# Performance work log

Hardware: AMD Instinct MI355X
Metric: run time of the kernel (lower is better)

Reference implementation:

```python
import jax, jax.numpy as jnp
import numpy as np

TEMPERATURE = 0.07
SIM_THRESHOLD = 0.5


def setup_inputs() -> dict:
    key = jax.random.key(0)
    k1, k2 = jax.random.split(key)
    features = jax.random.normal(k1, (4096, 2, 128), dtype=jnp.float32)
    labels = jax.random.randint(k2, (4096, 100), 0, 2).astype(jnp.float32)
    return {"features": features, "labels": labels}


def reference(features, labels):
    B, V, D = features.shape

    # label Jaccard similarity -> positive/negative masks [B, B]
    intersection = labels @ labels.T
    row_sum = jnp.sum(labels, axis=1, keepdims=True)
    union = row_sum + row_sum.T - intersection
    similarity = intersection / (union + 1e-6)
    positive_mask = (similarity >= SIM_THRESHOLD).astype(jnp.float32)
    negative_mask = 1.0 - positive_mask

    # torch.cat(torch.unbind(features, dim=1), dim=0) -> [V*B, D] (view-major)
    contrast_feature = jnp.transpose(features, (1, 0, 2)).reshape(V * B, D)
    dot_similarities = (contrast_feature @ contrast_feature.T) / TEMPERATURE  # [VB, VB]

    # numerical stability: subtract detached row max over the FULL row
    logits_max = jax.lax.stop_gradient(jnp.max(dot_similarities, axis=1, keepdims=True))
    logits = dot_similarities - logits_max

    # only the top-left [B, B] block is ever indexed by the original loop
    e = jnp.exp(logits[:B, :B])
    pos_sum = jnp.sum(e * positive_mask, axis=1)  # [B]
    neg_sum = jnp.sum(e * negative_mask, axis=1)  # [B]

    has_pos = jnp.sum(positive_mask, axis=1) > 0  # rows with >=1 positive
    pos_safe = jnp.where(has_pos, pos_sum, 1.0)
    den_safe = jnp.where(has_pos, pos_sum + neg_sum, 1.0)
    per_row = -jnp.log(pos_safe / den_safe)

    count = jnp.sum(has_pos.astype(jnp.float32))
    loss = jnp.sum(jnp.where(has_pos, per_row, 0.0)) / jnp.maximum(count, 1.0)
    return loss
```

## Files before the change

kernel.cpp:

```cpp
#include <hip/hip_runtime.h>
#include <math.h>

#define B_ROWS 4096
#define DIM 128
#define LBL 100
#define NCT 32

typedef __attribute__((ext_vector_type(8))) short bf16x8;
typedef __attribute__((ext_vector_type(4))) float f32x4;

__device__ __forceinline__ unsigned f2bf(float x) {
  union { float f; unsigned u; } a; a.f = x;
  unsigned r = a.u + 0x7fffu + ((a.u >> 16) & 1u);
  return r >> 16;
}

__device__ __forceinline__ void lds_dma16(void* l, const void* g) {
  __builtin_amdgcn_global_load_lds(
      (const __attribute__((address_space(1))) void*)g,
      (__attribute__((address_space(3))) void*)l, 16, 0, 0);
}

__global__ void pack_kernel(const float* __restrict__ feat,
                            uint4* __restrict__ cf,
                            float* __restrict__ accum) {
  if (blockIdx.x == 0 && threadIdx.x < 2) accum[threadIdx.x] = 0.0f;
  int g = blockIdx.x * 256 + threadIdx.x;
  int tile = g >> 11, rem = g & 2047;
  int r = rem >> 4, kc = rem & 15;
  const float* src = feat + ((size_t)(tile * 128 + r)) * 256 + kc * 8;
  float4 a = *(const float4*)src;
  float4 b = *(const float4*)(src + 4);
  uint4 ov;
  ov.x = f2bf(a.x) | (f2bf(a.y) << 16);
  ov.y = f2bf(a.z) | (f2bf(a.w) << 16);
  ov.z = f2bf(b.x) | (f2bf(b.y) << 16);
  ov.w = f2bf(b.z) | (f2bf(b.w) << 16);
  cf[(size_t)tile * 2048 + kc * 128 + (r ^ kc)] = ov;
}

__global__ void seedlabel_kernel(const float* __restrict__ feat,
                                 const float* __restrict__ labels,
                                 uint4* __restrict__ Lb,
                                 int* __restrict__ rsv,
                                 float* __restrict__ seedRaw) {
  int w = (int)((blockIdx.x * blockDim.x + threadIdx.x) >> 6);
  int lane = threadIdx.x & 63;
  const float2* src = (const float2*)(feat + (size_t)w * 256);
  float2 f = src[lane];
  float b0 = __uint_as_float(f2bf(f.x) << 16);
  float b1 = __uint_as_float(f2bf(f.y) << 16);
  float s = b0 * b0 + b1 * b1;
  #pragma unroll
  for (int off = 32; off >= 1; off >>= 1) s += __shfl_xor(s, off);
  float x0 = labels[(size_t)w * LBL + lane];
  float x1 = (lane < LBL - 64) ? labels[(size_t)w * LBL + 64 + lane] : 0.0f;
  unsigned long long m0 = __ballot(x0 != 0.0f);
  unsigned long long m1 = __ballot(x1 != 0.0f);
  if (lane == 0) {
    Lb[w] = make_uint4((unsigned)m0, (unsigned)(m0 >> 32),
                       (unsigned)m1, (unsigned)(m1 >> 32));
    rsv[w] = __popcll(m0) + __popcll(m1);
    seedRaw[w] = s - 0.15f;
  }
}

__launch_bounds__(256, 2)
__global__ void main_kernel(const uint4* __restrict__ cf,
                            const uint4* __restrict__ Lb,
                            const int* __restrict__ rsv,
                            const float* __restrict__ seedRaw,
                            float2* __restrict__ part) {
  __shared__ uint4 As[2048];
  __shared__ uint4 Bs[2048];
  __shared__ uint4 cLb[128];
  __shared__ uint4 rLb[128];
  __shared__ int   cRs[128];
  __shared__ int   rRs[128];
  __shared__ float sS[128];
  const int tid = threadIdx.x;
  const int lane = tid & 63;
  const int l15 = lane & 15;
  const int quad = lane >> 4;
  const int wave = tid >> 6;
  const int wi = (wave & 1) * 64;
  const int wj = (wave >> 1) * 64;
  const int rowBase = blockIdx.x * 128;
  const int colBase = blockIdx.y * 128;
  const float invT = 1.0f / 0.07f;

  #pragma unroll
  for (int it = 0; it < 8; ++it) {
    int flat = it * 256 + tid;
    lds_dma16(&As[flat], &cf[(size_t)blockIdx.x * 2048 + flat]);
    lds_dma16(&Bs[flat], &cf[(size_t)blockIdx.y * 2048 + flat]);
  }
  if (tid < 128) {
    cLb[tid] = Lb[colBase + tid];
    cRs[tid] = rsv[colBase + tid];
    sS[tid] = seedRaw[rowBase + tid];
  } else {
    int t = tid - 128;
    rLb[t] = Lb[rowBase + t];
    rRs[t] = rsv[rowBase + t];
  }
  __syncthreads();

  float srow[16];
  #pragma unroll
  for (int ti = 0; ti < 4; ++ti)
    #pragma unroll
    for (int r = 0; r < 4; ++r)
      srow[ti * 4 + r] = sS[wi + ti * 16 + quad * 4 + r];

  const bf16x8* Asv = (const bf16x8*)As;
  const bf16x8* Bsv = (const bf16x8*)Bs;

  f32x4 acc[4][4];
  #pragma unroll
  for (int ti = 0; ti < 4; ++ti)
    #pragma unroll
    for (int tj = 0; tj < 4; ++tj)
      acc[ti][tj] = (f32x4){0.f, 0.f, 0.f, 0.f};

  #pragma unroll
  for (int ks = 0; ks < 4; ++ks) {
    const int kc = ks * 4 + quad;
    const int abase = kc * 128 + wi + (l15 ^ kc);
    const int bbase = kc * 128 + wj + (l15 ^ kc);
    bf16x8 af[4], bfr[4];
    #pragma unroll
    for (int t = 0; t < 4; ++t) {
      af[t] = Asv[abase + t * 16];
      bfr[t] = Bsv[bbase + t * 16];
    }
    #pragma unroll
    for (int ti = 0; ti < 4; ++ti)
      #pragma unroll
      for (int tj = 0; tj < 4; ++tj)
        acc[ti][tj] = __builtin_amdgcn_mfma_f32_16x16x32_bf16(
            af[ti], bfr[tj], acc[ti][tj], 0, 0, 0);
  }

  float p_s[16], n_s[16];
  #pragma unroll
  for (int i = 0; i < 16; ++i) { p_s[i] = 0.f; n_s[i] = 0.f; }
  #pragma unroll
  for (int ti = 0; ti < 4; ++ti)
    #pragma unroll
    for (int r = 0; r < 4; ++r) {
      int si = ti * 4 + r;
      float l0 = acc[ti][0][r], l1 = acc[ti][1][r];
      float l2 = acc[ti][2][r], l3 = acc[ti][3][r];
      float tm = fmaxf(fmaxf(l0, l1), fmaxf(l2, l3));
      if (tm > srow[si] - 6.3f) {
        int lrow = wi + ti * 16 + quad * 4 + r;
        uint4 la = rLb[lrow];
        int ra = rRs[lrow];
        float p = 0.f, n = 0.f;
        float lv[4] = {l0, l1, l2, l3};
        #pragma unroll
        for (int tj = 0; tj < 4; ++tj) {
          float e = __expf((lv[tj] - srow[si]) * invT);
          int lcol = wj + tj * 16 + l15;
          uint4 lb = cLb[lcol];
          int inter = __popc(la.x & lb.x) + __popc(la.y & lb.y) +
                      __popc(la.z & lb.z) + __popc(la.w & lb.w);
          if (3 * inter > ra + cRs[lcol]) p += e; else n += e;
        }
        p_s[si] = p;
        n_s[si] = n;
      }
    }

  #pragma unroll
  for (int si = 0; si < 16; ++si) {
    float p = p_s[si], n = n_s[si];
    #pragma unroll
    for (int off = 8; off >= 1; off >>= 1) {
      p += __shfl_xor(p, off);
      n += __shfl_xor(n, off);
    }
    p_s[si] = p;
    n_s[si] = n;
  }

  __syncthreads();
  float* mbuf = (float*)As;
  if (wj == 64 && l15 == 0) {
    #pragma unroll
    for (int ti = 0; ti < 4; ++ti)
      #pragma unroll
      for (int r = 0; r < 4; ++r) {
        int row = wi + ti * 16 + quad * 4 + r;
        int si = ti * 4 + r;
        mbuf[row * 2 + 0] = p_s[si];
        mbuf[row * 2 + 1] = n_s[si];
      }
  }
  __syncthreads();
  if (wj == 0 && l15 == 0) {
    #pragma unroll
    for (int ti = 0; ti < 4; ++ti)
      #pragma unroll
      for (int r = 0; r < 4; ++r) {
        int row = wi + ti * 16 + quad * 4 + r;
        int si = ti * 4 + r;
        float p = p_s[si] + mbuf[row * 2 + 0];
        float n = n_s[si] + mbuf[row * 2 + 1];
        part[(size_t)blockIdx.y * B_ROWS + rowBase + row] = make_float2(p, n);
      }
  }
}

__global__ void merge_kernel(const float2* __restrict__ part,
                             const int* __restrict__ rsv,
                             float* __restrict__ accum) {
  int row = blockIdx.x * 256 + threadIdx.x;
  float p = 0.f, n = 0.f;
  #pragma unroll
  for (int c = 0; c < NCT; ++c) {
    float2 v = part[(size_t)c * B_ROWS + row];
    p += v.x;
    n += v.y;
  }
  float per = 0.f, cnt = 0.f;
  if (rsv[row] > 0) {
    per = -logf(p / (p + n));
    cnt = 1.f;
  }
  #pragma unroll
  for (int off = 32; off >= 1; off >>= 1) {
    per += __shfl_xor(per, off);
    cnt += __shfl_xor(cnt, off);
  }
  if ((threadIdx.x & 63) == 0) {
    atomicAdd(accum + 0, per);
    atomicAdd(accum + 1, cnt);
  }
}

__global__ void fin_kernel(const float* __restrict__ accum,
                           float* __restrict__ out) {
  out[0] = accum[0] / fmaxf(accum[1], 1.0f);
}

extern "C" void kernel_launch(void* const* d_in, const int* in_sizes, int n_in,
                              void* d_out, int out_size, void* d_ws, size_t ws_size,
                              hipStream_t stream) {
  const float* feat = (const float*)d_in[0];
  const float* labels = (const float*)d_in[1];
  float* out = (float*)d_out;
  char* ws = (char*)d_ws;
  uint4* cf = (uint4*)(ws + 0);
  uint4* Lbm = (uint4*)(ws + 1048576);
  int* rsv = (int*)(ws + 1114112);
  float* seedRaw = (float*)(ws + 1130496);
  float2* part = (float2*)(ws + 1146880);
  float* accum = (float*)(ws + 1146880 + 1048576);

  hipLaunchKernelGGL(pack_kernel, dim3(256), dim3(256), 0, stream,
                     feat, cf, accum);
  hipLaunchKernelGGL(seedlabel_kernel, dim3(1024), dim3(256), 0, stream,
                     feat, labels, Lbm, rsv, seedRaw);
  hipLaunchKernelGGL(main_kernel, dim3(NCT, NCT), dim3(256), 0, stream,
                     cf, Lbm, rsv, seedRaw, part);
  hipLaunchKernelGGL(merge_kernel, dim3(B_ROWS / 256), dim3(256), 0, stream,
                     part, rsv, accum);
  hipLaunchKernelGGL(fin_kernel, dim3(1), dim3(1), 0, stream, accum, out);
}
```

Measured before the change: 85.01 us.

## Exploit Gram symmetry with triangular tile grid and fuse bf16 packing into main kernel

The main kernel now launches only the upper-triangular 528 tile pairs of the symmetric Gram matrix and computes both row-wise and column-wise exp sums from each off-diagonal tile, writing partials for both row blocks. The separate pack kernel is removed; each block converts fp32 features to swizzled bf16 in LDS itself and computes the squared-norm seeds from the LDS data. This roughly halves the MFMA work and removes a kernel launch and its intermediate buffer. In exchange, each tile does more exp and popcount work and loads fp32 from global with conversion instead of using async LDS DMA, and the triangular index decode adds a small loop.

```diff
diff --git a/kernel.cpp b/kernel.cpp
--- a/kernel.cpp
+++ b/kernel.cpp
@@ -2,9 +2,9 @@
 #include <math.h>
 
 #define B_ROWS 4096
-#define DIM 128
 #define LBL 100
 #define NCT 32
+#define NTRI 528
 
 typedef __attribute__((ext_vector_type(8))) short bf16x8;
 typedef __attribute__((ext_vector_type(4))) float f32x4;
@@ -14,45 +14,17 @@
   unsigned r = a.u + 0x7fffu + ((a.u >> 16) & 1u);
   return r >> 16;
 }
-
-__device__ __forceinline__ void lds_dma16(void* l, const void* g) {
-  __builtin_amdgcn_global_load_lds(
-      (const __attribute__((address_space(1))) void*)g,
-      (__attribute__((address_space(3))) void*)l, 16, 0, 0);
-}
-
-__global__ void pack_kernel(const float* __restrict__ feat,
-                            uint4* __restrict__ cf,
-                            float* __restrict__ accum) {
+__device__ __forceinline__ float bf2f(unsigned h) {
+  return __uint_as_float(h << 16);
+}
+
+__global__ void label_kernel(const float* __restrict__ labels,
+                             uint4* __restrict__ Lb,
+                             int* __restrict__ rsv,
+                             float* __restrict__ accum) {
   if (blockIdx.x == 0 && threadIdx.x < 2) accum[threadIdx.x] = 0.0f;
-  int g = blockIdx.x * 256 + threadIdx.x;
-  int tile = g >> 11, rem = g & 2047;
-  int r = rem >> 4, kc = rem & 15;
-  const float* src = feat + ((size_t)(tile * 128 + r)) * 256 + kc * 8;
-  float4 a = *(const float4*)src;
-  float4 b = *(const float4*)(src + 4);
-  uint4 ov;
-  ov.x = f2bf(a.x) | (f2bf(a.y) << 16);
-  ov.y = f2bf(a.z) | (f2bf(a.w) << 16);
-  ov.z = f2bf(b.x) | (f2bf(b.y) << 16);
-  ov.w = f2bf(b.z) | (f2bf(b.w) << 16);
-  cf[(size_t)tile * 2048 + kc * 128 + (r ^ kc)] = ov;
-}
-
-__global__ void seedlabel_kernel(const float* __restrict__ feat,
-                                 const float* __restrict__ labels,
-                                 uint4* __restrict__ Lb,
-                                 int* __restrict__ rsv,
-                                 float* __restrict__ seedRaw) {
   int w = (int)((blockIdx.x * blockDim.x + threadIdx.x) >> 6);
   int lane = threadIdx.x & 63;
-  const float2* src = (const float2*)(feat + (size_t)w * 256);
-  float2 f = src[lane];
-  float b0 = __uint_as_float(f2bf(f.x) << 16);
-  float b1 = __uint_as_float(f2bf(f.y) << 16);
-  float s = b0 * b0 + b1 * b1;
-  #pragma unroll
-  for (int off = 32; off >= 1; off >>= 1) s += __shfl_xor(s, off);
   float x0 = labels[(size_t)w * LBL + lane];
   float x1 = (lane < LBL - 64) ? labels[(size_t)w * LBL + 64 + lane] : 0.0f;
   unsigned long long m0 = __ballot(x0 != 0.0f);
@@ -61,23 +33,26 @@
     Lb[w] = make_uint4((unsigned)m0, (unsigned)(m0 >> 32),
                        (unsigned)m1, (unsigned)(m1 >> 32));
     rsv[w] = __popcll(m0) + __popcll(m1);
-    seedRaw[w] = s - 0.15f;
   }
 }
 
 __launch_bounds__(256, 2)
-__global__ void main_kernel(const uint4* __restrict__ cf,
+__global__ void main_kernel(const float* __restrict__ feat,
                             const uint4* __restrict__ Lb,
                             const int* __restrict__ rsv,
-                            const float* __restrict__ seedRaw,
                             float2* __restrict__ part) {
   __shared__ uint4 As[2048];
   __shared__ uint4 Bs[2048];
-  __shared__ uint4 cLb[128];
-  __shared__ uint4 rLb[128];
-  __shared__ int   cRs[128];
-  __shared__ int   rRs[128];
-  __shared__ float sS[128];
+  __shared__ uint4 rLbS[128], cLbS[128];
+  __shared__ int rRsS[128], cRsS[128];
+  __shared__ float sS[128], sB[128];
+
+  int bid = blockIdx.x;
+  int bx = 0, off = 0;
+  while (bid >= off + (NCT - bx)) { off += NCT - bx; ++bx; }
+  int by = bx + (bid - off);
+  const bool diag = (bx == by);
+
   const int tid = threadIdx.x;
   const int lane = tid & 63;
   const int l15 = lane & 15;
@@ -85,33 +60,73 @@
   const int wave = tid >> 6;
   const int wi = (wave & 1) * 64;
   const int wj = (wave >> 1) * 64;
-  const int rowBase = blockIdx.x * 128;
-  const int colBase = blockIdx.y * 128;
+  const int rowBase = bx * 128;
+  const int colBase = by * 128;
   const float invT = 1.0f / 0.07f;
 
   #pragma unroll
   for (int it = 0; it < 8; ++it) {
     int flat = it * 256 + tid;
-    lds_dma16(&As[flat], &cf[(size_t)blockIdx.x * 2048 + flat]);
-    lds_dma16(&Bs[flat], &cf[(size_t)blockIdx.y * 2048 + flat]);
+    int r = flat >> 4, kc = flat & 15;
+    const float* pa = feat + (size_t)(rowBase + r) * 256 + kc * 8;
+    float4 a0 = *(const float4*)pa;
+    float4 a1 = *(const float4*)(pa + 4);
+    uint4 av;
+    av.x = f2bf(a0.x) | (f2bf(a0.y) << 16);
+    av.y = f2bf(a0.z) | (f2bf(a0.w) << 16);
+    av.z = f2bf(a1.x) | (f2bf(a1.y) << 16);
+    av.w = f2bf(a1.z) | (f2bf(a1.w) << 16);
+    As[kc * 128 + (r ^ kc)] = av;
+    const float* pb = feat + (size_t)(colBase + r) * 256 + kc * 8;
+    float4 b0 = *(const float4*)pb;
+    float4 b1 = *(const float4*)(pb + 4);
+    uint4 bv;
+    bv.x = f2bf(b0.x) | (f2bf(b0.y) << 16);
+    bv.y = f2bf(b0.z) | (f2bf(b0.w) << 16);
+    bv.z = f2bf(b1.x) | (f2bf(b1.y) << 16);
+    bv.w = f2bf(b1.z) | (f2bf(b1.w) << 16);
+    Bs[kc * 128 + (r ^ kc)] = bv;
   }
   if (tid < 128) {
-    cLb[tid] = Lb[colBase + tid];
-    cRs[tid] = rsv[colBase + tid];
-    sS[tid] = seedRaw[rowBase + tid];
+    cLbS[tid] = Lb[colBase + tid];
+    cRsS[tid] = rsv[colBase + tid];
   } else {
     int t = tid - 128;
-    rLb[t] = Lb[rowBase + t];
-    rRs[t] = rsv[rowBase + t];
+    rLbS[t] = Lb[rowBase + t];
+    rRsS[t] = rsv[rowBase + t];
   }
   __syncthreads();
 
-  float srow[16];
+  {
+    int t = tid & 127;
+    const uint4* src = (tid < 128) ? As : Bs;
+    float s = 0.f;
+    #pragma unroll
+    for (int kc = 0; kc < 16; ++kc) {
+      uint4 c = src[kc * 128 + (t ^ kc)];
+      float v;
+      v = bf2f(c.x & 0xffffu); s += v * v;
+      v = bf2f(c.x >> 16);     s += v * v;
+      v = bf2f(c.y & 0xffffu); s += v * v;
+      v = bf2f(c.y >> 16);     s += v * v;
+      v = bf2f(c.z & 0xffffu); s += v * v;
+      v = bf2f(c.z >> 16);     s += v * v;
+      v = bf2f(c.w & 0xffffu); s += v * v;
+      v = bf2f(c.w >> 16);     s += v * v;
+    }
+    if (tid < 128) sS[t] = s - 0.15f;
+    else sB[t] = s - 0.15f;
+  }
+  __syncthreads();
+
+  float srow[16], scol[4];
   #pragma unroll
   for (int ti = 0; ti < 4; ++ti)
     #pragma unroll
     for (int r = 0; r < 4; ++r)
       srow[ti * 4 + r] = sS[wi + ti * 16 + quad * 4 + r];
+  #pragma unroll
+  for (int tj = 0; tj < 4; ++tj) scol[tj] = sB[wj + tj * 16 + l15];
 
   const bf16x8* Asv = (const bf16x8*)As;
   const bf16x8* Bsv = (const bf16x8*)Bs;
@@ -142,9 +157,12 @@
             af[ti], bfr[tj], acc[ti][tj], 0, 0, 0);
   }
 
-  float p_s[16], n_s[16];
+  float p_s[16], n_s[16], cp[4], cn[4], cmax[4];
   #pragma unroll
   for (int i = 0; i < 16; ++i) { p_s[i] = 0.f; n_s[i] = 0.f; }
+  #pragma unroll
+  for (int tj = 0; tj < 4; ++tj) { cp[tj] = 0.f; cn[tj] = 0.f; cmax[tj] = -1e30f; }
+
   #pragma unroll
   for (int ti = 0; ti < 4; ++ti)
     #pragma unroll
@@ -152,41 +170,79 @@
       int si = ti * 4 + r;
       float l0 = acc[ti][0][r], l1 = acc[ti][1][r];
       float l2 = acc[ti][2][r], l3 = acc[ti][3][r];
+      cmax[0] = fmaxf(cmax[0], l0);
+      cmax[1] = fmaxf(cmax[1], l1);
+      cmax[2] = fmaxf(cmax[2], l2);
+      cmax[3] = fmaxf(cmax[3], l3);
       float tm = fmaxf(fmaxf(l0, l1), fmaxf(l2, l3));
       if (tm > srow[si] - 6.3f) {
         int lrow = wi + ti * 16 + quad * 4 + r;
-        uint4 la = rLb[lrow];
-        int ra = rRs[lrow];
-        float p = 0.f, n = 0.f;
+        uint4 la = rLbS[lrow];
+        int ra = rRsS[lrow];
+        float p = p_s[si], n = n_s[si];
         float lv[4] = {l0, l1, l2, l3};
         #pragma unroll
         for (int tj = 0; tj < 4; ++tj) {
           float e = __expf((lv[tj] - srow[si]) * invT);
           int lcol = wj + tj * 16 + l15;
-          uint4 lb = cLb[lcol];
+          uint4 lb = cLbS[lcol];
           int inter = __popc(la.x & lb.x) + __popc(la.y & lb.y) +
                       __popc(la.z & lb.z) + __popc(la.w & lb.w);
-          if (3 * inter > ra + cRs[lcol]) p += e; else n += e;
+          if (3 * inter > ra + cRsS[lcol]) p += e; else n += e;
         }
         p_s[si] = p;
         n_s[si] = n;
       }
     }
 
+  if (!diag) {
+    #pragma unroll
+    for (int tj = 0; tj < 4; ++tj) {
+      if (cmax[tj] > scol[tj] - 6.3f) {
+        int lcol = wj + tj * 16 + l15;
+        uint4 lb = cLbS[lcol];
+        int rb = cRsS[lcol];
+        float p = cp[tj], n = cn[tj];
+        #pragma unroll
+        for (int ti = 0; ti < 4; ++ti)
+          #pragma unroll
+          for (int r = 0; r < 4; ++r) {
+            float e = __expf((acc[ti][tj][r] - scol[tj]) * invT);
+            int lrow = wi + ti * 16 + quad * 4 + r;
+            uint4 la = rLbS[lrow];
+            int inter = __popc(la.x & lb.x) + __popc(la.y & lb.y) +
+                        __popc(la.z & lb.z) + __popc(la.w & lb.w);
+            if (3 * inter > rRsS[lrow] + rb) p += e; else n += e;
+          }
+        cp[tj] = p;
+        cn[tj] = n;
+      }
+    }
+  }
+
   #pragma unroll
   for (int si = 0; si < 16; ++si) {
     float p = p_s[si], n = n_s[si];
     #pragma unroll
-    for (int off = 8; off >= 1; off >>= 1) {
-      p += __shfl_xor(p, off);
-      n += __shfl_xor(n, off);
+    for (int o = 8; o >= 1; o >>= 1) {
+      p += __shfl_xor(p, o);
+      n += __shfl_xor(n, o);
     }
     p_s[si] = p;
     n_s[si] = n;
   }
+  #pragma unroll
+  for (int tj = 0; tj < 4; ++tj) {
+    float p = cp[tj], n = cn[tj];
+    p += __shfl_xor(p, 16); n += __shfl_xor(n, 16);
+    p += __shfl_xor(p, 32); n += __shfl_xor(n, 32);
+    cp[tj] = p;
+    cn[tj] = n;
+  }
 
   __syncthreads();
-  float* mbuf = (float*)As;
+  float* mrow = (float*)As;
+  float* mcol = ((float*)As) + 256;
   if (wj == 64 && l15 == 0) {
     #pragma unroll
     for (int ti = 0; ti < 4; ++ti)
@@ -194,9 +250,17 @@
       for (int r = 0; r < 4; ++r) {
         int row = wi + ti * 16 + quad * 4 + r;
         int si = ti * 4 + r;
-        mbuf[row * 2 + 0] = p_s[si];
-        mbuf[row * 2 + 1] = n_s[si];
+        mrow[row * 2 + 0] = p_s[si];
+        mrow[row * 2 + 1] = n_s[si];
       }
+  }
+  if (!diag && wi == 64 && quad == 0) {
+    #pragma unroll
+    for (int tj = 0; tj < 4; ++tj) {
+      int col = wj + tj * 16 + l15;
+      mcol[col * 2 + 0] = cp[tj];
+      mcol[col * 2 + 1] = cn[tj];
+    }
   }
   __syncthreads();
   if (wj == 0 && l15 == 0) {
@@ -206,10 +270,19 @@
       for (int r = 0; r < 4; ++r) {
         int row = wi + ti * 16 + quad * 4 + r;
         int si = ti * 4 + r;
-        float p = p_s[si] + mbuf[row * 2 + 0];
-        float n = n_s[si] + mbuf[row * 2 + 1];
-        part[(size_t)blockIdx.y * B_ROWS + rowBase + row] = make_float2(p, n);
+        float p = p_s[si] + mrow[row * 2 + 0];
+        float n = n_s[si] + mrow[row * 2 + 1];
+        part[(size_t)by * B_ROWS + rowBase + row] = make_float2(p, n);
       }
+  }
+  if (!diag && wi == 0 && quad == 0) {
+    #pragma unroll
+    for (int tj = 0; tj < 4; ++tj) {
+      int col = wj + tj * 16 + l15;
+      float p = cp[tj] + mcol[col * 2 + 0];
+      float n = cn[tj] + mcol[col * 2 + 1];
+      part[(size_t)bx * B_ROWS + colBase + col] = make_float2(p, n);
+    }
   }
 }
 
@@ -230,9 +303,9 @@
     cnt = 1.f;
   }
   #pragma unroll
-  for (int off = 32; off >= 1; off >>= 1) {
-    per += __shfl_xor(per, off);
-    cnt += __shfl_xor(cnt, off);
+  for (int o = 32; o >= 1; o >>= 1) {
+    per += __shfl_xor(per, o);
+    cnt += __shfl_xor(cnt, o);
   }
   if ((threadIdx.x & 63) == 0) {
     atomicAdd(accum + 0, per);
@@ -252,19 +325,15 @@
   const float* labels = (const float*)d_in[1];
   float* out = (float*)d_out;
   char* ws = (char*)d_ws;
-  uint4* cf = (uint4*)(ws + 0);
-  uint4* Lbm = (uint4*)(ws + 1048576);
-  int* rsv = (int*)(ws + 1114112);
-  float* seedRaw = (float*)(ws + 1130496);
-  float2* part = (float2*)(ws + 1146880);
-  float* accum = (float*)(ws + 1146880 + 1048576);
-
-  hipLaunchKernelGGL(pack_kernel, dim3(256), dim3(256), 0, stream,
-                     feat, cf, accum);
-  hipLaunchKernelGGL(seedlabel_kernel, dim3(1024), dim3(256), 0, stream,
-                     feat, labels, Lbm, rsv, seedRaw);
-  hipLaunchKernelGGL(main_kernel, dim3(NCT, NCT), dim3(256), 0, stream,
-                     cf, Lbm, rsv, seedRaw, part);
+  uint4* Lbm = (uint4*)(ws + 0);
+  int* rsv = (int*)(ws + 65536);
+  float2* part = (float2*)(ws + 81920);
+  float* accum = (float*)(ws + 81920 + 1048576);
+
+  hipLaunchKernelGGL(label_kernel, dim3(1024), dim3(256), 0, stream,
+                     labels, Lbm, rsv, accum);
+  hipLaunchKernelGGL(main_kernel, dim3(NTRI), dim3(256), 0, stream,
+                     feat, Lbm, rsv, part);
   hipLaunchKernelGGL(merge_kernel, dim3(B_ROWS / 256), dim3(256), 0, stream,
                      part, rsv, accum);
   hipLaunchKernelGGL(fin_kernel, dim3(1), dim3(1), 0, stream, accum, out);
```

Result: faster. 82.94 us (-2.4%).
